# Performance work log

Measured on AMD Instinct MI355X. Metric: run time of the kernel, lower is better.

The kernel has to match this reference:

```python
import jax, jax.numpy as jnp
import numpy as np

N_NODES = 100000
N_EDGES = 3200000  # avg degree 32
EPS = 1e-12


def setup_inputs() -> dict:
    key = jax.random.key(0)
    k1, k2, k3, k4, k5 = jax.random.split(key, 5)
    positions = jax.random.normal(k1, (N_NODES, 3), dtype=jnp.float32)
    node_feat = jnp.ones((N_NODES, 1), dtype=jnp.float32)  # dummy 1x0e data
    w0 = jax.random.normal(k2, (1,), dtype=jnp.float32)    # linear weight for 0e output
    w1 = jax.random.normal(k3, (3,), dtype=jnp.float32)    # linear weight for 1o output (elementwise)
    edge_src = jax.random.randint(k4, (N_EDGES,), 0, N_NODES, dtype=jnp.int32)
    edge_dst = jax.random.randint(k5, (N_EDGES,), 0, N_NODES, dtype=jnp.int32)
    return {"positions": positions, "node_feat": node_feat, "w0": w0, "w1": w1,
            "edge_src": edge_src, "edge_dst": edge_dst}


def reference(positions, node_feat, w0, w1, edge_src, edge_dst):
    n_nodes = positions.shape[0]
    # relative positions per edge: dest - src  [E,3]
    rel = positions[edge_dst] - positions[edge_src]
    # spherical harmonics lmax=1: Y0 = 1 (constant 0e), Y1 = unit direction (1o)
    norm = jnp.sqrt(jnp.sum(rel * rel, axis=-1, keepdims=True))
    sh1 = rel / jnp.maximum(norm, EPS)                      # [E,3]
    # gather dest-node scalar feature (code gathers dest_node_feat)
    s = node_feat[edge_dst]                                 # [E,1]
    # tensor product of 0e scalar with (0e + 1o): tp0 = s*1, tp1 = s*sh1
    # LinearLayer: elementwise multiply by per-irrep weight vectors
    out0 = w0 * s                                           # [E,1]
    out1 = w1 * (s * sh1)                                   # [E,3]
    edge_out = jnp.concatenate([out0, out1], axis=-1)       # [E,4]
    # scatter-mean aggregation over incoming edges per dest node
    sums = jax.ops.segment_sum(edge_out, edge_dst, num_segments=n_nodes)
    ones = jnp.ones((edge_out.shape[0], 1), dtype=edge_out.dtype)
    counts = jax.ops.segment_sum(ones, edge_dst, num_segments=n_nodes)
    return sums / jnp.maximum(counts, 1.0)                  # [N,4]
```

## Files before the change

kernel.cpp:

```cpp
#include <hip/hip_runtime.h>


#define EPS 1e-12f
#define FSCALE 128.0f
#define FBIAS 128
#define CHUNK_SHIFT 12
#define CHUNK 4096
#define NCHUNK_MAX 32
#define BLKA 512
#define TPA 4
#define BLKB 512
#define SUBS 12

__global__ void repack_pos(const float* __restrict__ pos,
                           float4* __restrict__ pos4, int n_nodes) {
    int n = blockIdx.x * blockDim.x + threadIdx.x;
    if (n >= n_nodes) return;
    float4 p;
    p.x = pos[3 * n + 0];
    p.y = pos[3 * n + 1];
    p.z = pos[3 * n + 2];
    p.w = 0.f;
    pos4[n] = p;
}

__device__ __forceinline__ unsigned long long make_rec(const float4* __restrict__ pos4,
                                                       int s, int d) {
    float4 pd = pos4[d];
    float4 ps = pos4[s];
    float rx = pd.x - ps.x;
    float ry = pd.y - ps.y;
    float rz = pd.z - ps.z;
    float nrm = sqrtf(rx * rx + ry * ry + rz * rz);
    float inv = 1.0f / fmaxf(nrm, EPS);
    unsigned fx = (unsigned)(FBIAS + (int)rintf(rx * inv * FSCALE));
    unsigned fy = (unsigned)(FBIAS + (int)rintf(ry * inv * FSCALE));
    unsigned fz = (unsigned)(FBIAS + (int)rintf(rz * inv * FSCALE));
    unsigned local = (unsigned)d & (CHUNK - 1);
    return ((unsigned long long)local << 27)
         | ((unsigned long long)fx << 18)
         | ((unsigned long long)fy << 9)
         | (unsigned long long)fz;
}

__global__ __launch_bounds__(BLKA) void phaseA(
        const float4* __restrict__ pos4,
        const int* __restrict__ dst,
        const int* __restrict__ src,
        unsigned* __restrict__ gcnt,
        unsigned long long* __restrict__ recs,
        int n_edges, int cap, int n_chunk) {
    __shared__ unsigned h[NCHUNK_MAX];
    __shared__ unsigned base[NCHUNK_MAX];
    int tid = threadIdx.x;
    if (tid < n_chunk) h[tid] = 0;
    __syncthreads();

    long e0 = (long)blockIdx.x * (BLKA * TPA);
    unsigned long long rec[TPA];
    int ch[TPA];
    unsigned rank[TPA];
    bool val[TPA];
#pragma unroll
    for (int t = 0; t < TPA; ++t) {
        long j = e0 + (long)t * BLKA + tid;
        val[t] = (j < n_edges);
        if (val[t]) {
            int d = dst[j];
            int s = src[j];
            ch[t] = d >> CHUNK_SHIFT;
            rec[t] = make_rec(pos4, s, d);
            rank[t] = atomicAdd(&h[ch[t]], 1u);
        }
    }
    __syncthreads();
    if (tid < n_chunk) base[tid] = h[tid] ? atomicAdd(&gcnt[tid], h[tid]) : 0u;
    __syncthreads();
#pragma unroll
    for (int t = 0; t < TPA; ++t) {
        if (val[t]) {
            unsigned idx = base[ch[t]] + rank[t];
            if (idx < (unsigned)cap)
                recs[(size_t)ch[t] * (unsigned)cap + idx] = rec[t];
        }
    }
}

__global__ __launch_bounds__(BLKB) void phaseB(
        const unsigned* __restrict__ gcnt,
        const unsigned long long* __restrict__ recs,
        unsigned long long* __restrict__ accR,
        int cap, int n_chunk, int padded) {
    __shared__ unsigned long long lds[CHUNK];
    int c   = (int)blockIdx.x % n_chunk;
    int sub = (int)blockIdx.x / n_chunk;
    unsigned cnt = gcnt[c];
    if (cnt > (unsigned)cap) cnt = (unsigned)cap;

    for (int i = threadIdx.x; i < CHUNK; i += BLKB) lds[i] = 0ull;
    __syncthreads();

    const unsigned long long* bucket = recs + (size_t)c * (unsigned)cap;
    for (unsigned j = sub * BLKB + threadIdx.x; j < cnt; j += SUBS * BLKB) {
        unsigned long long r = bucket[j];
        unsigned local = (unsigned)(r >> 27);
        unsigned long long p = (((r >> 18) & 511ull) << 48)
                             | (((r >>  9) & 511ull) << 32)
                             | (((r      ) & 511ull) << 16)
                             | 1ull;
        atomicAdd(&lds[local], p);
    }
    __syncthreads();

    unsigned long long* row = accR + (size_t)sub * (unsigned)padded
                                   + (size_t)c * CHUNK;
    for (int i = threadIdx.x; i < CHUNK; i += BLKB) row[i] = lds[i];
}

__global__ void finalize_binned(const unsigned long long* __restrict__ accR,
                                const float* __restrict__ feat,
                                const float* __restrict__ w0,
                                const float* __restrict__ w1,
                                float* __restrict__ out,
                                int n_nodes, int padded) {
    int n = blockIdx.x * blockDim.x + threadIdx.x;
    if (n >= n_nodes) return;
    int Fx = 0, Fy = 0, Fz = 0, C = 0;
    for (int s = 0; s < SUBS; ++s) {
        unsigned long long v = accR[(size_t)s * (unsigned)padded + (unsigned)n];
        Fx += (int)(v >> 48);
        Fy += (int)((v >> 32) & 0xffffull);
        Fz += (int)((v >> 16) & 0xffffull);
        C  += (int)(v & 0xffffull);
    }
    float c = (float)C;
    float rd = 1.0f / fmaxf(c, 1.0f);
    float sx = (float)Fx * (1.0f / FSCALE) - c;
    float sy = (float)Fy * (1.0f / FSCALE) - c;
    float sz = (float)Fz * (1.0f / FSCALE) - c;
    float f = feat[n];
    float4 o;
    o.x = w0[0] * f * c * rd;
    o.y = w1[0] * f * sx * rd;
    o.z = w1[1] * f * sy * rd;
    o.w = w1[2] * f * sz * rd;
    ((float4*)out)[n] = o;
}

__global__ void edge_kernel_agent(const float* __restrict__ pos,
                                  const int* __restrict__ dst,
                                  const int* __restrict__ src,
                                  unsigned long long* __restrict__ acc,
                                  int n_edges, int n_nodes, int rmask) {
    int i = blockIdx.x * blockDim.x + threadIdx.x;
    if (i >= n_edges) return;
    int s = src[i];
    int d = dst[i];
    float rx = pos[3 * d + 0] - pos[3 * s + 0];
    float ry = pos[3 * d + 1] - pos[3 * s + 1];
    float rz = pos[3 * d + 2] - pos[3 * s + 2];
    float nrm = sqrtf(rx * rx + ry * ry + rz * rz);
    float inv = 1.0f / fmaxf(nrm, EPS);
    unsigned fx = (unsigned)(FBIAS + (int)rintf(rx * inv * FSCALE));
    unsigned fy = (unsigned)(FBIAS + (int)rintf(ry * inv * FSCALE));
    unsigned fz = (unsigned)(FBIAS + (int)rintf(rz * inv * FSCALE));
    unsigned long long p = ((unsigned long long)fx << 48)
                         | ((unsigned long long)fy << 32)
                         | ((unsigned long long)fz << 16) | 1ull;
    unsigned r = (unsigned)blockIdx.x & (unsigned)rmask;
    atomicAdd(acc + (size_t)r * (unsigned)n_nodes + (unsigned)d, p);
}

__global__ void finalize_flat(const unsigned long long* __restrict__ acc,
                              const float* __restrict__ feat,
                              const float* __restrict__ w0,
                              const float* __restrict__ w1,
                              float* __restrict__ out,
                              int n_nodes, int R) {
    int n = blockIdx.x * blockDim.x + threadIdx.x;
    if (n >= n_nodes) return;
    int Fx = 0, Fy = 0, Fz = 0, C = 0;
    for (int r = 0; r < R; ++r) {
        unsigned long long v = acc[(size_t)r * n_nodes + n];
        Fx += (int)(v >> 48);
        Fy += (int)((v >> 32) & 0xffffull);
        Fz += (int)((v >> 16) & 0xffffull);
        C  += (int)(v & 0xffffull);
    }
    float c = (float)C;
    float rd = 1.0f / fmaxf(c, 1.0f);
    float sx = (float)Fx * (1.0f / FSCALE) - c;
    float sy = (float)Fy * (1.0f / FSCALE) - c;
    float sz = (float)Fz * (1.0f / FSCALE) - c;
    float f = feat[n];
    float4 o;
    o.x = w0[0] * f * c * rd;
    o.y = w1[0] * f * sx * rd;
    o.z = w1[1] * f * sy * rd;
    o.w = w1[2] * f * sz * rd;
    ((float4*)out)[n] = o;
}

extern "C" void kernel_launch(void* const* d_in, const int* in_sizes, int n_in,
                              void* d_out, int out_size, void* d_ws, size_t ws_size,
                              hipStream_t stream) {
    const float* pos  = (const float*)d_in[0];
    const float* feat = (const float*)d_in[1];
    const float* w0   = (const float*)d_in[2];
    const float* w1   = (const float*)d_in[3];
    const int* esrc   = (const int*)d_in[4];
    const int* edst   = (const int*)d_in[5];
    int n_nodes = in_sizes[0] / 3;
    int n_edges = in_sizes[4];

    int n_chunk = (n_nodes + CHUNK - 1) >> CHUNK_SHIFT;
    int padded  = n_chunk * CHUNK;
    int cap = (int)((long)n_edges * CHUNK / n_nodes + 8192);

    size_t off_pos4 = 0;
    size_t pos4_bytes = (size_t)padded * sizeof(float4);
    size_t off_gcnt = (pos4_bytes + 255) & ~(size_t)255;
    size_t off_recs = off_gcnt + 256;
    size_t recs_bytes = (size_t)n_chunk * (unsigned)cap * sizeof(unsigned long long);
    size_t off_accR = off_recs + ((recs_bytes + 255) & ~(size_t)255);
    size_t accR_bytes = (size_t)SUBS * (unsigned)padded * sizeof(unsigned long long);
    size_t need = off_accR + accR_bytes;

    int nb = 256;
    int ng = (n_nodes + nb - 1) / nb;

    if (n_chunk <= NCHUNK_MAX && ws_size >= need) {
        float4* pos4 = (float4*)((char*)d_ws + off_pos4);
        unsigned* gcnt = (unsigned*)((char*)d_ws + off_gcnt);
        unsigned long long* recs = (unsigned long long*)((char*)d_ws + off_recs);
        unsigned long long* accR = (unsigned long long*)((char*)d_ws + off_accR);

        hipMemsetAsync(gcnt, 0, (size_t)n_chunk * sizeof(unsigned), stream);
        repack_pos<<<ng, nb, 0, stream>>>(pos, pos4, n_nodes);

        int ga = (int)((n_edges + (long)BLKA * TPA - 1) / ((long)BLKA * TPA));
        phaseA<<<ga, BLKA, 0, stream>>>(pos4, edst, esrc, gcnt, recs,
                                        n_edges, cap, n_chunk);
        phaseB<<<n_chunk * SUBS, BLKB, 0, stream>>>(gcnt, recs, accR,
                                                    cap, n_chunk, padded);
        finalize_binned<<<ng, nb, 0, stream>>>(accR, feat, w0, w1,
                                               (float*)d_out, n_nodes, padded);
    } else {
        int R = 4;
        while (R > 1 && (size_t)R * n_nodes * sizeof(unsigned long long) > ws_size) R >>= 1;
        unsigned long long* acc = (unsigned long long*)d_ws;
        hipMemsetAsync(acc, 0, (size_t)R * n_nodes * sizeof(unsigned long long), stream);
        int eb = 256;
        int eg = (n_edges + eb - 1) / eb;
        edge_kernel_agent<<<eg, eb, 0, stream>>>(pos, edst, esrc, acc,
                                                 n_edges, n_nodes, R - 1);
        finalize_flat<<<ng, nb, 0, stream>>>(acc, feat, w0, w1,
                                             (float*)d_out, n_nodes, R);
    }
}
```

Before: 137.3 us.

## Fuse repack, binning, chunk accumulation and finalize into one cooperative kernel

Replaces the memset plus four separate launches (position repack, edge binning, per-chunk LDS accumulation, finalize) with a single cooperative kernel of 512 blocks. The phases are separated by grid-wide syncs, and each block loops over a contiguous slice of edges. The number of accumulation sub-partitions is now derived from the grid size rather than fixed, and bucket capacity is recomputed to match. This is meant to remove per-launch overhead and inter-kernel gaps. In exchange it adds grid-sync cost and fewer resident blocks for the latency-bound edge gather phase, and it relies on all 512 blocks being co-resident.

```diff
diff --git a/kernel.cpp b/kernel.cpp
--- a/kernel.cpp
+++ b/kernel.cpp
@@ -1,4 +1,7 @@
 #include <hip/hip_runtime.h>
+#include <hip/hip_cooperative_groups.h>
+
+namespace cg = cooperative_groups;
 
 
 #define EPS 1e-12f
@@ -7,144 +10,142 @@
 #define CHUNK_SHIFT 12
 #define CHUNK 4096
 #define NCHUNK_MAX 32
-#define BLKA 512
+#define BLK 512
 #define TPA 4
-#define BLKB 512
-#define SUBS 12
-
-__global__ void repack_pos(const float* __restrict__ pos,
-                           float4* __restrict__ pos4, int n_nodes) {
-    int n = blockIdx.x * blockDim.x + threadIdx.x;
-    if (n >= n_nodes) return;
-    float4 p;
-    p.x = pos[3 * n + 0];
-    p.y = pos[3 * n + 1];
-    p.z = pos[3 * n + 2];
-    p.w = 0.f;
-    pos4[n] = p;
-}
-
-__device__ __forceinline__ unsigned long long make_rec(const float4* __restrict__ pos4,
-                                                       int s, int d) {
-    float4 pd = pos4[d];
-    float4 ps = pos4[s];
-    float rx = pd.x - ps.x;
-    float ry = pd.y - ps.y;
-    float rz = pd.z - ps.z;
-    float nrm = sqrtf(rx * rx + ry * ry + rz * rz);
-    float inv = 1.0f / fmaxf(nrm, EPS);
-    unsigned fx = (unsigned)(FBIAS + (int)rintf(rx * inv * FSCALE));
-    unsigned fy = (unsigned)(FBIAS + (int)rintf(ry * inv * FSCALE));
-    unsigned fz = (unsigned)(FBIAS + (int)rintf(rz * inv * FSCALE));
-    unsigned local = (unsigned)d & (CHUNK - 1);
-    return ((unsigned long long)local << 27)
-         | ((unsigned long long)fx << 18)
-         | ((unsigned long long)fy << 9)
-         | (unsigned long long)fz;
-}
-
-__global__ __launch_bounds__(BLKA) void phaseA(
-        const float4* __restrict__ pos4,
+#define GRID 512
+
+__global__ __launch_bounds__(BLK, 4) void fused_all(
+        const float* __restrict__ pos,
         const int* __restrict__ dst,
         const int* __restrict__ src,
+        const float* __restrict__ feat,
+        const float* __restrict__ w0,
+        const float* __restrict__ w1,
+        float4* __restrict__ pos4,
         unsigned* __restrict__ gcnt,
         unsigned long long* __restrict__ recs,
-        int n_edges, int cap, int n_chunk) {
+        unsigned long long* __restrict__ accR,
+        float* __restrict__ out,
+        int n_nodes, int n_edges, int n_chunk, int cap, int padded, int subs) {
+    cg::grid_group grid = cg::this_grid();
+    __shared__ unsigned long long lds[CHUNK];
     __shared__ unsigned h[NCHUNK_MAX];
-    __shared__ unsigned base[NCHUNK_MAX];
-    int tid = threadIdx.x;
-    if (tid < n_chunk) h[tid] = 0;
-    __syncthreads();
-
-    long e0 = (long)blockIdx.x * (BLKA * TPA);
-    unsigned long long rec[TPA];
-    int ch[TPA];
-    unsigned rank[TPA];
-    bool val[TPA];
+    __shared__ unsigned hb[NCHUNK_MAX];
+    const int tid = threadIdx.x;
+    const int b = blockIdx.x;
+
+    const int n = b * BLK + tid;
+    if (n < n_nodes) {
+        float4 p;
+        p.x = pos[3 * n + 0];
+        p.y = pos[3 * n + 1];
+        p.z = pos[3 * n + 2];
+        p.w = 0.f;
+        pos4[n] = p;
+    }
+    if (b == 0 && tid < n_chunk) gcnt[tid] = 0;
+    grid.sync();
+
+    {
+        long e0 = (long)n_edges * b / GRID;
+        long e1 = (long)n_edges * (b + 1) / GRID;
+        for (long base_e = e0; base_e < e1; base_e += (long)BLK * TPA) {
+            if (tid < n_chunk) h[tid] = 0;
+            __syncthreads();
+            unsigned long long rec[TPA];
+            int ch[TPA];
+            unsigned rank[TPA];
+            bool val[TPA];
 #pragma unroll
-    for (int t = 0; t < TPA; ++t) {
-        long j = e0 + (long)t * BLKA + tid;
-        val[t] = (j < n_edges);
-        if (val[t]) {
-            int d = dst[j];
-            int s = src[j];
-            ch[t] = d >> CHUNK_SHIFT;
-            rec[t] = make_rec(pos4, s, d);
-            rank[t] = atomicAdd(&h[ch[t]], 1u);
+            for (int t = 0; t < TPA; ++t) {
+                long j = base_e + (long)t * BLK + tid;
+                val[t] = (j < e1);
+                if (val[t]) {
+                    int d = dst[j];
+                    int s = src[j];
+                    float4 pd = pos4[d];
+                    float4 ps = pos4[s];
+                    float rx = pd.x - ps.x;
+                    float ry = pd.y - ps.y;
+                    float rz = pd.z - ps.z;
+                    float inv = 1.0f / fmaxf(sqrtf(rx * rx + ry * ry + rz * rz), EPS);
+                    unsigned fx = (unsigned)(FBIAS + (int)rintf(rx * inv * FSCALE));
+                    unsigned fy = (unsigned)(FBIAS + (int)rintf(ry * inv * FSCALE));
+                    unsigned fz = (unsigned)(FBIAS + (int)rintf(rz * inv * FSCALE));
+                    unsigned local = (unsigned)d & (CHUNK - 1);
+                    ch[t] = d >> CHUNK_SHIFT;
+                    rec[t] = ((unsigned long long)local << 27)
+                           | ((unsigned long long)fx << 18)
+                           | ((unsigned long long)fy << 9)
+                           | (unsigned long long)fz;
+                    rank[t] = atomicAdd(&h[ch[t]], 1u);
+                }
+            }
+            __syncthreads();
+            if (tid < n_chunk && h[tid]) hb[tid] = atomicAdd(&gcnt[tid], h[tid]);
+            __syncthreads();
+#pragma unroll
+            for (int t = 0; t < TPA; ++t) {
+                if (val[t]) {
+                    unsigned idx = hb[ch[t]] + rank[t];
+                    if (idx < (unsigned)cap)
+                        recs[(size_t)ch[t] * (unsigned)cap + idx] = rec[t];
+                }
+            }
+            __syncthreads();
         }
     }
-    __syncthreads();
-    if (tid < n_chunk) base[tid] = h[tid] ? atomicAdd(&gcnt[tid], h[tid]) : 0u;
-    __syncthreads();
-#pragma unroll
-    for (int t = 0; t < TPA; ++t) {
-        if (val[t]) {
-            unsigned idx = base[ch[t]] + rank[t];
-            if (idx < (unsigned)cap)
-                recs[(size_t)ch[t] * (unsigned)cap + idx] = rec[t];
+    grid.sync();
+
+    {
+        int c = b % n_chunk;
+        int sub = b / n_chunk;
+        if (sub < subs) {
+            for (int i = tid; i < CHUNK; i += BLK) lds[i] = 0ull;
+            __syncthreads();
+            unsigned cnt = gcnt[c];
+            if (cnt > (unsigned)cap) cnt = (unsigned)cap;
+            const unsigned long long* bucket = recs + (size_t)c * (unsigned)cap;
+            for (unsigned j = (unsigned)sub * BLK + tid; j < cnt;
+                 j += (unsigned)subs * BLK) {
+                unsigned long long r = bucket[j];
+                unsigned local = (unsigned)(r >> 27);
+                unsigned long long p = (((r >> 18) & 511ull) << 48)
+                                     | (((r >>  9) & 511ull) << 32)
+                                     | (((r      ) & 511ull) << 16)
+                                     | 1ull;
+                atomicAdd(&lds[local], p);
+            }
+            __syncthreads();
+            unsigned long long* row = accR + (size_t)sub * (unsigned)padded
+                                           + (size_t)c * CHUNK;
+            for (int i = tid; i < CHUNK; i += BLK) row[i] = lds[i];
         }
     }
-}
-
-__global__ __launch_bounds__(BLKB) void phaseB(
-        const unsigned* __restrict__ gcnt,
-        const unsigned long long* __restrict__ recs,
-        unsigned long long* __restrict__ accR,
-        int cap, int n_chunk, int padded) {
-    __shared__ unsigned long long lds[CHUNK];
-    int c   = (int)blockIdx.x % n_chunk;
-    int sub = (int)blockIdx.x / n_chunk;
-    unsigned cnt = gcnt[c];
-    if (cnt > (unsigned)cap) cnt = (unsigned)cap;
-
-    for (int i = threadIdx.x; i < CHUNK; i += BLKB) lds[i] = 0ull;
-    __syncthreads();
-
-    const unsigned long long* bucket = recs + (size_t)c * (unsigned)cap;
-    for (unsigned j = sub * BLKB + threadIdx.x; j < cnt; j += SUBS * BLKB) {
-        unsigned long long r = bucket[j];
-        unsigned local = (unsigned)(r >> 27);
-        unsigned long long p = (((r >> 18) & 511ull) << 48)
-                             | (((r >>  9) & 511ull) << 32)
-                             | (((r      ) & 511ull) << 16)
-                             | 1ull;
-        atomicAdd(&lds[local], p);
-    }
-    __syncthreads();
-
-    unsigned long long* row = accR + (size_t)sub * (unsigned)padded
-                                   + (size_t)c * CHUNK;
-    for (int i = threadIdx.x; i < CHUNK; i += BLKB) row[i] = lds[i];
-}
-
-__global__ void finalize_binned(const unsigned long long* __restrict__ accR,
-                                const float* __restrict__ feat,
-                                const float* __restrict__ w0,
-                                const float* __restrict__ w1,
-                                float* __restrict__ out,
-                                int n_nodes, int padded) {
-    int n = blockIdx.x * blockDim.x + threadIdx.x;
-    if (n >= n_nodes) return;
-    int Fx = 0, Fy = 0, Fz = 0, C = 0;
-    for (int s = 0; s < SUBS; ++s) {
-        unsigned long long v = accR[(size_t)s * (unsigned)padded + (unsigned)n];
-        Fx += (int)(v >> 48);
-        Fy += (int)((v >> 32) & 0xffffull);
-        Fz += (int)((v >> 16) & 0xffffull);
-        C  += (int)(v & 0xffffull);
-    }
-    float c = (float)C;
-    float rd = 1.0f / fmaxf(c, 1.0f);
-    float sx = (float)Fx * (1.0f / FSCALE) - c;
-    float sy = (float)Fy * (1.0f / FSCALE) - c;
-    float sz = (float)Fz * (1.0f / FSCALE) - c;
-    float f = feat[n];
-    float4 o;
-    o.x = w0[0] * f * c * rd;
-    o.y = w1[0] * f * sx * rd;
-    o.z = w1[1] * f * sy * rd;
-    o.w = w1[2] * f * sz * rd;
-    ((float4*)out)[n] = o;
+    grid.sync();
+
+    if (n < n_nodes) {
+        int Fx = 0, Fy = 0, Fz = 0, C = 0;
+        for (int s2 = 0; s2 < subs; ++s2) {
+            unsigned long long v = accR[(size_t)s2 * (unsigned)padded + (unsigned)n];
+            Fx += (int)(v >> 48);
+            Fy += (int)((v >> 32) & 0xffffull);
+            Fz += (int)((v >> 16) & 0xffffull);
+            C  += (int)(v & 0xffffull);
+        }
+        float c = (float)C;
+        float rd = 1.0f / fmaxf(c, 1.0f);
+        float sx = (float)Fx * (1.0f / FSCALE) - c;
+        float sy = (float)Fy * (1.0f / FSCALE) - c;
+        float sz = (float)Fz * (1.0f / FSCALE) - c;
+        float f = feat[n];
+        float4 o;
+        o.x = w0[0] * f * c * rd;
+        o.y = w1[0] * f * sx * rd;
+        o.z = w1[1] * f * sy * rd;
+        o.w = w1[2] * f * sz * rd;
+        ((float4*)out)[n] = o;
+    }
 }
 
 __global__ void edge_kernel_agent(const float* __restrict__ pos,
@@ -215,7 +216,8 @@
 
     int n_chunk = (n_nodes + CHUNK - 1) >> CHUNK_SHIFT;
     int padded  = n_chunk * CHUNK;
-    int cap = (int)((long)n_edges * CHUNK / n_nodes + 8192);
+    int subs    = GRID / n_chunk;
+    int cap = (int)((long)n_edges / n_chunk + 16384);
 
     size_t off_pos4 = 0;
     size_t pos4_bytes = (size_t)padded * sizeof(float4);
@@ -223,28 +225,26 @@
     size_t off_recs = off_gcnt + 256;
     size_t recs_bytes = (size_t)n_chunk * (unsigned)cap * sizeof(unsigned long long);
     size_t off_accR = off_recs + ((recs_bytes + 255) & ~(size_t)255);
-    size_t accR_bytes = (size_t)SUBS * (unsigned)padded * sizeof(unsigned long long);
+    size_t accR_bytes = (size_t)subs * (unsigned)padded * sizeof(unsigned long long);
     size_t need = off_accR + accR_bytes;
 
     int nb = 256;
     int ng = (n_nodes + nb - 1) / nb;
 
-    if (n_chunk <= NCHUNK_MAX && ws_size >= need) {
+    if (n_chunk <= NCHUNK_MAX && subs >= 4 && ws_size >= need) {
         float4* pos4 = (float4*)((char*)d_ws + off_pos4);
         unsigned* gcnt = (unsigned*)((char*)d_ws + off_gcnt);
         unsigned long long* recs = (unsigned long long*)((char*)d_ws + off_recs);
         unsigned long long* accR = (unsigned long long*)((char*)d_ws + off_accR);
 
-        hipMemsetAsync(gcnt, 0, (size_t)n_chunk * sizeof(unsigned), stream);
-        repack_pos<<<ng, nb, 0, stream>>>(pos, pos4, n_nodes);
-
-        int ga = (int)((n_edges + (long)BLKA * TPA - 1) / ((long)BLKA * TPA));
-        phaseA<<<ga, BLKA, 0, stream>>>(pos4, edst, esrc, gcnt, recs,
-                                        n_edges, cap, n_chunk);
-        phaseB<<<n_chunk * SUBS, BLKB, 0, stream>>>(gcnt, recs, accR,
-                                                    cap, n_chunk, padded);
-        finalize_binned<<<ng, nb, 0, stream>>>(accR, feat, w0, w1,
-                                               (float*)d_out, n_nodes, padded);
+        void* args[] = { (void*)&pos, (void*)&edst, (void*)&esrc,
+                         (void*)&feat, (void*)&w0, (void*)&w1,
+                         (void*)&pos4, (void*)&gcnt, (void*)&recs,
+                         (void*)&accR, (void*)&d_out,
+                         (void*)&n_nodes, (void*)&n_edges, (void*)&n_chunk,
+                         (void*)&cap, (void*)&padded, (void*)&subs };
+        hipLaunchCooperativeKernel((void*)fused_all, dim3(GRID), dim3(BLK),
+                                   args, 0, stream);
     } else {
         int R = 4;
         while (R > 1 && (size_t)R * n_nodes * sizeof(unsigned long long) > ws_size) R >>= 1;
```

Result: slower. 315.8 us (+130.1%).
